# Kernel tuning notes

Measured on AMD Instinct MI355X. Metric: run time of the kernel, lower is better.

The kernel has to match this reference:

```python
import jax, jax.numpy as jnp
import numpy as np

N, INPUT_DIM, DIM, K, M_BOOK = 8192, 256, 128, 8192, 8
EPS = 1e-5  # torch BatchNorm1d default eps


def _bn(h, g, b, rm, rv):
    # eval-mode BatchNorm1d with running stats (dropout is identity in eval)
    return (h - rm) / jnp.sqrt(rv + EPS) * g + b


def setup_inputs() -> dict:
    key = jax.random.key(0)
    ks = jax.random.split(key, 20)
    s = 0.02
    inp = {
        "x": jax.random.normal(ks[0], (N, INPUT_DIM), jnp.float32),
        # encoder: input_dim -> 128 -> 256 -> dim
        "W1": jax.random.normal(ks[1], (INPUT_DIM, 128), jnp.float32) * s,
        "b1": jnp.zeros((128,), jnp.float32),
        "g1": jnp.ones((128,), jnp.float32),
        "be1": jnp.zeros((128,), jnp.float32),
        "rm1": jax.random.normal(ks[2], (128,), jnp.float32) * 0.1,
        "rv1": jax.random.uniform(ks[3], (128,), jnp.float32, 0.5, 1.5),
        "W2": jax.random.normal(ks[4], (128, 256), jnp.float32) * s,
        "b2": jnp.zeros((256,), jnp.float32),
        "g2": jnp.ones((256,), jnp.float32),
        "be2": jnp.zeros((256,), jnp.float32),
        "rm2": jax.random.normal(ks[5], (256,), jnp.float32) * 0.1,
        "rv2": jax.random.uniform(ks[6], (256,), jnp.float32, 0.5, 1.5),
        "W3": jax.random.normal(ks[7], (256, DIM), jnp.float32) * s,
        "b3": jnp.zeros((DIM,), jnp.float32),
        # m_book codebooks, torch init uniform(-1/K, 1/K)
        "codebooks": jax.random.uniform(ks[8], (M_BOOK, K, DIM), jnp.float32, -1.0 / K, 1.0 / K),
        # decoder: dim -> 256 -> 128 -> input_dim
        "W4": jax.random.normal(ks[9], (DIM, 256), jnp.float32) * s,
        "b4": jnp.zeros((256,), jnp.float32),
        "g3": jnp.ones((256,), jnp.float32),
        "be3": jnp.zeros((256,), jnp.float32),
        "rm3": jax.random.normal(ks[10], (256,), jnp.float32) * 0.1,
        "rv3": jax.random.uniform(ks[11], (256,), jnp.float32, 0.5, 1.5),
        "W5": jax.random.normal(ks[12], (256, 128), jnp.float32) * s,
        "b5": jnp.zeros((128,), jnp.float32),
        "g4": jnp.ones((128,), jnp.float32),
        "be4": jnp.zeros((128,), jnp.float32),
        "rm4": jax.random.normal(ks[13], (128,), jnp.float32) * 0.1,
        "rv4": jax.random.uniform(ks[14], (128,), jnp.float32, 0.5, 1.5),
        "W6": jax.random.normal(ks[15], (128, INPUT_DIM), jnp.float32) * s,
        "b6": jnp.zeros((INPUT_DIM,), jnp.float32),
    }
    return inp


def reference(x, W1, b1, g1, be1, rm1, rv1, W2, b2, g2, be2, rm2, rv2, W3, b3,
              codebooks, W4, b4, g3, be3, rm3, rv3, W5, b5, g4, be4, rm4, rv4, W6, b6):
    # encoder
    h = jax.nn.relu(_bn(x @ W1 + b1, g1, be1, rm1, rv1))
    h = jax.nn.relu(_bn(h @ W2 + b2, g2, be2, rm2, rv2))
    ze = h @ W3 + b3  # [N, DIM]

    # residual VQ over m_book codebooks
    def step(res, E):  # res [N, C], E [K, C]
        # squared distance ||e - r||^2 = ||r||^2 - 2 r.e + ||e||^2 (no [N,K,C] broadcast)
        d = (jnp.sum(res * res, axis=1, keepdims=True)
             - 2.0 * (res @ E.T)
             + jnp.sum(E * E, axis=1)[None, :])  # [N, K]
        idx = jnp.argmin(d, axis=1)  # [N]
        ce = E[idx]  # [N, C]
        return res - ce, (res, ce)

    _, (res_s, ce_s) = jax.lax.scan(step, ze, codebooks)  # each [M_BOOK, N, DIM]
    zq = jnp.sum(ce_s, axis=0)  # [N, DIM]

    # straight-through estimator
    di = ze + jax.lax.stop_gradient(zq - ze)

    # decoder
    h = jax.nn.relu(_bn(di @ W4 + b4, g3, be3, rm3, rv3))
    h = jax.nn.relu(_bn(h @ W5 + b5, g4, be4, rm4, rv4))
    x_hat = h @ W6 + b6  # [N, INPUT_DIM]
    return x_hat, res_s, ce_s
```

## Files before the change

### kernel.cpp

```cpp
#include <hip/hip_runtime.h>
#include <hip/hip_bf16.h>


typedef __bf16 bf16x8 __attribute__((ext_vector_type(8)));
typedef float  f32x4  __attribute__((ext_vector_type(4)));
typedef unsigned short ushort8v __attribute__((ext_vector_type(8)));

#define MFMA16(a,b,c) __builtin_amdgcn_mfma_f32_16x16x32_bf16((a),(b),(c),0,0,0)

__device__ __forceinline__ float b2f(ushort u){ return __uint_as_float(((unsigned)u) << 16); }
__device__ __forceinline__ ushort f2b_rne(float x){
  unsigned u = __float_as_uint(x);
  return (ushort)((u + 0x7fffu + ((u >> 16) & 1u)) >> 16);
}

__device__ __forceinline__ void cvt8(const float* p, bf16x8& h8, bf16x8& l8){
  f32x4 v0 = *(const f32x4*)p;
  f32x4 v1 = *(const f32x4*)(p + 4);
  ushort8v uh, ul;
  #pragma unroll
  for (int i = 0; i < 4; i++){
    float a = v0[i]; ushort h = f2b_rne(a); uh[i] = h;     ul[i]     = f2b_rne(a - b2f(h));
    float b = v1[i]; ushort g = f2b_rne(b); uh[i + 4] = g; ul[i + 4] = f2b_rne(b - b2f(g));
  }
  h8 = __builtin_bit_cast(bf16x8, uh);
  l8 = __builtin_bit_cast(bf16x8, ul);
}

template<int KK, int NN, bool HAS_BLO>
__device__ __forceinline__ f32x4 dotct(const bf16x8* ah, const bf16x8* al,
                                       const ushort* __restrict__ Bfh,
                                       const ushort* __restrict__ Bfl,
                                       int ct, int L){
  constexpr int KS = KK / 32, CT = NN / 16;
  f32x4 acc = {0.f, 0.f, 0.f, 0.f};
  #pragma unroll
  for (int ks = 0; ks < KS; ks++){
    int bo = ((ks * CT + ct) * 64 + L) * 8;
    bf16x8 bh = *(const bf16x8*)(Bfh + bo);
    acc = MFMA16(ah[ks], bh, acc);
    acc = MFMA16(al[ks], bh, acc);
    if constexpr (HAS_BLO){
      bf16x8 bl = *(const bf16x8*)(Bfl + bo);
      acc = MFMA16(ah[ks], bl, acc);
    }
  }
  return acc;
}

__device__ __forceinline__ void ebook_body(const float* __restrict__ Ef, ushort* __restrict__ Eb,
                                           float* __restrict__ hen, int code, int L){
  float2 e2 = *(const float2*)(Ef + code * 128 + L * 2);
  ushort h0 = f2b_rne(e2.x), h1 = f2b_rne(e2.y);
  int d = L * 2;
  int o = ((((code >> 4) * 4 + (d >> 5)) * 4 + ((d >> 3) & 3)) * 16 + (code & 15)) * 8 + (d & 7);
  *(unsigned*)(Eb + o) = (unsigned)h0 | ((unsigned)h1 << 16);
  float eh0 = b2f(h0), eh1 = b2f(h1);
  float s = eh0 * eh0 + eh1 * eh1;
  #pragma unroll
  for (int mask = 1; mask <= 32; mask <<= 1) s += __shfl_xor(s, mask);
  if (L == 0) hen[code] = 0.5f * s;
}

__device__ __forceinline__ void swz_body(const float* __restrict__ Wm, ushort* __restrict__ Wfh,
                                         ushort* __restrict__ Wfl, int N, int b){
  int gid = b * 256 + threadIdx.x;
  int k = gid / N, n = gid - k * N;
  int kt = k >> 5, kr = k & 31, nt = n >> 4, nr = n & 15;
  int lane = (kr >> 3) * 16 + nr, tt = kr & 7;
  int o = (((kt * (N >> 4)) + nt) * 64 + lane) * 8 + tt;
  float v = Wm[gid];
  ushort h = f2b_rne(v);
  Wfh[o] = h;
  if (Wfl) Wfl[o] = f2b_rne(v - b2f(h));
}

__global__ __launch_bounds__(256) void k_prep(
    const float* __restrict__ W1, const float* __restrict__ W2, const float* __restrict__ W3,
    const float* __restrict__ W4, const float* __restrict__ W5, const float* __restrict__ W6,
    ushort* W1fh, ushort* W1fl, ushort* W2fh, ushort* W2fl, ushort* W3fh, ushort* W3fl,
    ushort* W4fh, ushort* W5fh, ushort* W6fh,
    const float* __restrict__ CB, ushort* __restrict__ Eb, float* __restrict__ hen,
    const float* g1,const float* be1,const float* rm1,const float* rv1,
    const float* g2,const float* be2,const float* rm2,const float* rv2,
    const float* g3,const float* be3,const float* rm3,const float* rv3,
    const float* g4,const float* be4,const float* rm4,const float* rv4,
    float* s1,float* t1,float* s2,float* t2,float* s3,float* t3,float* s4,float* t4)
{
  int b = blockIdx.x;
  if (b < 768){
    if      (b < 128) swz_body(W1, W1fh, W1fl, 128, b);
    else if (b < 256) swz_body(W2, W2fh, W2fl, 256, b - 128);
    else if (b < 384) swz_body(W3, W3fh, W3fl, 128, b - 256);
    else if (b < 512) swz_body(W4, W4fh, nullptr, 256, b - 384);
    else if (b < 640) swz_body(W5, W5fh, nullptr, 128, b - 512);
    else              swz_body(W6, W6fh, nullptr, 256, b - 640);
  } else if (b == 768){
    int t = threadIdx.x;
    if (t < 128){
      float sa = g1[t] / sqrtf(rv1[t] + 1e-5f);
      s1[t] = sa; t1[t] = be1[t] - rm1[t] * sa;
      float sb = g4[t] / sqrtf(rv4[t] + 1e-5f);
      s4[t] = sb; t4[t] = be4[t] - rm4[t] * sb;
    }
    if (t < 256){
      float sa = g2[t] / sqrtf(rv2[t] + 1e-5f);
      s2[t] = sa; t2[t] = be2[t] - rm2[t] * sa;
      float sb = g3[t] / sqrtf(rv3[t] + 1e-5f);
      s3[t] = sb; t3[t] = be3[t] - rm3[t] * sb;
    }
  } else {
    ebook_body(CB, Eb, hen, (b - 769) * 4 + (threadIdx.x >> 6), threadIdx.x & 63);
  }
}

__global__ __launch_bounds__(256) void k_encoder(
    const float* __restrict__ x,
    const ushort* __restrict__ W1fh, const ushort* __restrict__ W1fl,
    const ushort* __restrict__ W2fh, const ushort* __restrict__ W2fl,
    const ushort* __restrict__ W3fh, const ushort* __restrict__ W3fl,
    const float* __restrict__ b1, const float* __restrict__ s1, const float* __restrict__ t1,
    const float* __restrict__ b2, const float* __restrict__ s2, const float* __restrict__ t2,
    const float* __restrict__ b3,
    ushort* __restrict__ rhi, float* __restrict__ res)
{
  __shared__ __align__(16) float sA[16 * 260];
  __shared__ __align__(16) float sB[16 * 132];
  int tid = threadIdx.x;
  int wv = tid >> 6, L = tid & 63;
  int qd = L >> 4, c16 = L & 15;
  int row0 = blockIdx.x * 16;

  bf16x8 a1h[8], a1l[8];
  #pragma unroll
  for (int ks = 0; ks < 8; ks++)
    cvt8(x + (row0 + c16) * 256 + ks * 32 + qd * 8, a1h[ks], a1l[ks]);

  #pragma unroll
  for (int u = 0; u < 2; u++){
    int ct = wv * 2 + u;
    f32x4 acc = dotct<256,128,true>(a1h, a1l, W1fh, W1fl, ct, L);
    int col = ct * 16 + c16;
    float bia = b1[col], sc = s1[col], sh = t1[col];
    #pragma unroll
    for (int i = 0; i < 4; i++){
      float v = (acc[i] + bia) * sc + sh;
      sB[(qd * 4 + i) * 132 + col] = fmaxf(v, 0.f);
    }
  }
  __syncthreads();

  bf16x8 a2h[4], a2l[4];
  #pragma unroll
  for (int ks = 0; ks < 4; ks++)
    cvt8(sB + c16 * 132 + ks * 32 + qd * 8, a2h[ks], a2l[ks]);

  #pragma unroll
  for (int u = 0; u < 4; u++){
    int ct = wv * 4 + u;
    f32x4 acc = dotct<128,256,true>(a2h, a2l, W2fh, W2fl, ct, L);
    int col = ct * 16 + c16;
    float bia = b2[col], sc = s2[col], sh = t2[col];
    #pragma unroll
    for (int i = 0; i < 4; i++){
      float v = (acc[i] + bia) * sc + sh;
      sA[(qd * 4 + i) * 260 + col] = fmaxf(v, 0.f);
    }
  }
  __syncthreads();

  bf16x8 a3h[8], a3l[8];
  #pragma unroll
  for (int ks = 0; ks < 8; ks++)
    cvt8(sA + c16 * 260 + ks * 32 + qd * 8, a3h[ks], a3l[ks]);

  #pragma unroll
  for (int u = 0; u < 2; u++){
    int ct = wv * 2 + u;
    f32x4 acc = dotct<256,128,true>(a3h, a3l, W3fh, W3fl, ct, L);
    int col = ct * 16 + c16;
    float bia = b3[col];
    #pragma unroll
    for (int i = 0; i < 4; i++){
      int row = row0 + qd * 4 + i;
      float v = acc[i] + bia;
      int o = row * 128 + col;
      res[o] = v;
      rhi[o] = f2b_rne(v);
    }
  }
}

__global__ __launch_bounds__(256) void k_decoder(
    const ushort* __restrict__ dhi, const ushort* __restrict__ dlo,
    const ushort* __restrict__ W4fh, const ushort* __restrict__ W5fh,
    const ushort* __restrict__ W6fh,
    const float* __restrict__ b4, const float* __restrict__ s3, const float* __restrict__ t3,
    const float* __restrict__ b5, const float* __restrict__ s4, const float* __restrict__ t4,
    const float* __restrict__ b6,
    float* __restrict__ xhat)
{
  __shared__ __align__(16) float sA[16 * 260];
  __shared__ __align__(16) float sB[16 * 132];
  int tid = threadIdx.x;
  int wv = tid >> 6, L = tid & 63;
  int qd = L >> 4, c16 = L & 15;
  int row0 = blockIdx.x * 16;

  bf16x8 a1h[4], a1l[4];
  #pragma unroll
  for (int ks = 0; ks < 4; ks++){
    int off = (row0 + c16) * 128 + ks * 32 + qd * 8;
    a1h[ks] = *(const bf16x8*)(dhi + off);
    a1l[ks] = *(const bf16x8*)(dlo + off);
  }

  #pragma unroll
  for (int u = 0; u < 4; u++){
    int ct = wv * 4 + u;
    f32x4 acc = dotct<128,256,false>(a1h, a1l, W4fh, nullptr, ct, L);
    int col = ct * 16 + c16;
    float bia = b4[col], sc = s3[col], sh = t3[col];
    #pragma unroll
    for (int i = 0; i < 4; i++){
      float v = (acc[i] + bia) * sc + sh;
      sA[(qd * 4 + i) * 260 + col] = fmaxf(v, 0.f);
    }
  }
  __syncthreads();

  bf16x8 a2h[8], a2l[8];
  #pragma unroll
  for (int ks = 0; ks < 8; ks++)
    cvt8(sA + c16 * 260 + ks * 32 + qd * 8, a2h[ks], a2l[ks]);

  #pragma unroll
  for (int u = 0; u < 2; u++){
    int ct = wv * 2 + u;
    f32x4 acc = dotct<256,128,false>(a2h, a2l, W5fh, nullptr, ct, L);
    int col = ct * 16 + c16;
    float bia = b5[col], sc = s4[col], sh = t4[col];
    #pragma unroll
    for (int i = 0; i < 4; i++){
      float v = (acc[i] + bia) * sc + sh;
      sB[(qd * 4 + i) * 132 + col] = fmaxf(v, 0.f);
    }
  }
  __syncthreads();

  bf16x8 a3h[4], a3l[4];
  #pragma unroll
  for (int ks = 0; ks < 4; ks++)
    cvt8(sB + c16 * 132 + ks * 32 + qd * 8, a3h[ks], a3l[ks]);

  #pragma unroll
  for (int u = 0; u < 4; u++){
    int ct = wv * 4 + u;
    f32x4 acc = dotct<128,256,false>(a3h, a3l, W6fh, nullptr, ct, L);
    int col = ct * 16 + c16;
    float bia = b6[col];
    #pragma unroll
    for (int i = 0; i < 4; i++)
      xhat[(row0 + qd * 4 + i) * 256 + col] = acc[i] + bia;
  }
}

__global__ __launch_bounds__(256, 4) void k_vq_argmin(
  const ushort* __restrict__ Rhi,
  const ushort* __restrict__ Eb, const float* __restrict__ hen,
  float* __restrict__ cq, int* __restrict__ cj)
{
  __shared__ __align__(16) ushort etile[2][8192];
  __shared__ float henl[512];
  int rb = blockIdx.x & 63, ch = blockIdx.x >> 6;
  int tid = threadIdx.x;
  int wv = tid >> 6, L = tid & 63;
  int qd = L >> 4, c16 = L & 15;
  int row0 = rb * 128 + wv * 32;

  bf16x8 ah[2][4];
  #pragma unroll
  for (int t = 0; t < 2; t++){
    int r = row0 + t * 16 + c16;
    #pragma unroll
    for (int ks = 0; ks < 4; ks++)
      ah[t][ks] = *(const bf16x8*)(Rhi + r * 128 + ks * 32 + qd * 8);
  }
  henl[tid] = hen[ch * 512 + tid];
  henl[tid + 256] = hen[ch * 512 + 256 + tid];

  float best[2][4]; int bj[2][4];
  #pragma unroll
  for (int t = 0; t < 2; t++)
    #pragma unroll
    for (int i = 0; i < 4; i++){ best[t][i] = -3.0e38f; bj[t][i] = 0; }

  const ushort* ebc = Eb + (size_t)ch * 65536;
  int jb = ch * 512 + c16;

  {
    const ushort* src = ebc + tid * 8;
    f32x4 v0 = *(const f32x4*)(src + 0 * 2048);
    f32x4 v1 = *(const f32x4*)(src + 1 * 2048);
    f32x4 v2 = *(const f32x4*)(src + 2 * 2048);
    f32x4 v3 = *(const f32x4*)(src + 3 * 2048);
    *(f32x4*)(etile[0] + 0 * 2048 + tid * 8) = v0;
    *(f32x4*)(etile[0] + 1 * 2048 + tid * 8) = v1;
    *(f32x4*)(etile[0] + 2 * 2048 + tid * 8) = v2;
    *(f32x4*)(etile[0] + 3 * 2048 + tid * 8) = v3;
  }
  __syncthreads();

  #pragma unroll 1
  for (int tile = 0; tile < 8; ++tile){
    int cur = tile & 1;
    f32x4 v0, v1, v2, v3;
    if (tile < 7){
      const ushort* src = ebc + (tile + 1) * 8192 + tid * 8;
      v0 = *(const f32x4*)(src + 0 * 2048);
      v1 = *(const f32x4*)(src + 1 * 2048);
      v2 = *(const f32x4*)(src + 2 * 2048);
      v3 = *(const f32x4*)(src + 3 * 2048);
    }
    const ushort* lb = etile[cur];
    #pragma unroll
    for (int g = 0; g < 4; ++g){
      const ushort* gp = lb + g * 2048 + L * 8;
      bf16x8 b0 = *(const bf16x8*)(gp + 0);
      bf16x8 b1 = *(const bf16x8*)(gp + 512);
      bf16x8 b2 = *(const bf16x8*)(gp + 1024);
      bf16x8 b3 = *(const bf16x8*)(gp + 1536);
      int gg = tile * 4 + g;
      float mh = -henl[gg * 16 + c16];
      f32x4 a0 = {mh, mh, mh, mh}, a1 = {mh, mh, mh, mh};
      __builtin_amdgcn_s_setprio(1);
      a0 = MFMA16(ah[0][0], b0, a0); a1 = MFMA16(ah[1][0], b0, a1);
      a0 = MFMA16(ah[0][1], b1, a0); a1 = MFMA16(ah[1][1], b1, a1);
      a0 = MFMA16(ah[0][2], b2, a0); a1 = MFMA16(ah[1][2], b2, a1);
      a0 = MFMA16(ah[0][3], b3, a0); a1 = MFMA16(ah[1][3], b3, a1);
      __builtin_amdgcn_s_setprio(0);
      int jc = jb + gg * 16;
      #pragma unroll
      for (int i = 0; i < 4; i++){
        if (a0[i] > best[0][i]){ best[0][i] = a0[i]; bj[0][i] = jc; }
        if (a1[i] > best[1][i]){ best[1][i] = a1[i]; bj[1][i] = jc; }
      }
    }
    if (tile < 7){
      ushort* nb = etile[cur ^ 1];
      *(f32x4*)(nb + 0 * 2048 + tid * 8) = v0;
      *(f32x4*)(nb + 1 * 2048 + tid * 8) = v1;
      *(f32x4*)(nb + 2 * 2048 + tid * 8) = v2;
      *(f32x4*)(nb + 3 * 2048 + tid * 8) = v3;
    }
    __syncthreads();
  }

  #pragma unroll
  for (int mask = 1; mask <= 8; mask <<= 1){
    #pragma unroll
    for (int t = 0; t < 2; t++)
      #pragma unroll
      for (int i = 0; i < 4; i++){
        float ob = __shfl_xor(best[t][i], mask);
        int   oj = __shfl_xor(bj[t][i], mask);
        if (ob > best[t][i] || (ob == best[t][i] && oj < bj[t][i])){ best[t][i] = ob; bj[t][i] = oj; }
      }
  }
  if (c16 == 0){
    #pragma unroll
    for (int t = 0; t < 2; t++)
      #pragma unroll
      for (int i = 0; i < 4; i++){
        int r = row0 + t * 16 + qd * 4 + i;
        cq[r * 16 + ch] = best[t][i];
        cj[r * 16 + ch] = bj[t][i];
      }
  }
}

template<bool LAST>
__global__ __launch_bounds__(256) void k_vq_update(
  const float* __restrict__ cq, const int* __restrict__ cj,
  const float* __restrict__ Ef, const float* __restrict__ Efn,
  ushort* __restrict__ Eb, float* __restrict__ hen,
  float* __restrict__ res, const float* __restrict__ ze_s,
  ushort* __restrict__ rhi, ushort* __restrict__ rlo,
  float* __restrict__ res_s, float* __restrict__ ce_s)
{
  int idx = blockIdx.x * 4 + (threadIdx.x >> 6);
  int L = threadIdx.x & 63;
  int c = L & 15;
  float bq = cq[idx * 16 + c]; int bi = cj[idx * 16 + c];
  #pragma unroll
  for (int mask = 1; mask <= 8; mask <<= 1){
    float ob = __shfl_xor(bq, mask);
    int   oj = __shfl_xor(bi, mask);
    if (ob > bq || (ob == bq && oj < bi)){ bq = ob; bi = oj; }
  }
  int o = idx * 128 + L * 2;
  float2 ce = *(const float2*)(Ef + bi * 128 + L * 2);
  float2 r2 = *(const float2*)(res + o);
  *(float2*)(res_s + o) = r2;
  *(float2*)(ce_s + o) = ce;
  float rn0 = r2.x - ce.x, rn1 = r2.y - ce.y;
  if constexpr (LAST){
    float2 z2 = *(const float2*)(ze_s + o);
    float d0 = z2.x - rn0, d1 = z2.y - rn1;
    ushort h0 = f2b_rne(d0), h1 = f2b_rne(d1);
    *(unsigned*)(rhi + o) = (unsigned)h0 | ((unsigned)h1 << 16);
    ushort l0 = f2b_rne(d0 - b2f(h0)), l1 = f2b_rne(d1 - b2f(h1));
    *(unsigned*)(rlo + o) = (unsigned)l0 | ((unsigned)l1 << 16);
  } else {
    res[o] = rn0; res[o + 1] = rn1;
    ushort h0 = f2b_rne(rn0), h1 = f2b_rne(rn1);
    *(unsigned*)(rhi + o) = (unsigned)h0 | ((unsigned)h1 << 16);
    ebook_body(Efn, Eb, hen, idx, L);
  }
}

extern "C" void kernel_launch(void* const* d_in, const int* in_sizes, int n_in,
                              void* d_out, int out_size, void* d_ws, size_t ws_size,
                              hipStream_t stream)
{
  const float* x   = (const float*)d_in[0];
  const float* W1  = (const float*)d_in[1];
  const float* b1  = (const float*)d_in[2];
  const float* g1  = (const float*)d_in[3];
  const float* be1 = (const float*)d_in[4];
  const float* rm1 = (const float*)d_in[5];
  const float* rv1 = (const float*)d_in[6];
  const float* W2  = (const float*)d_in[7];
  const float* b2  = (const float*)d_in[8];
  const float* g2  = (const float*)d_in[9];
  const float* be2 = (const float*)d_in[10];
  const float* rm2 = (const float*)d_in[11];
  const float* rv2 = (const float*)d_in[12];
  const float* W3  = (const float*)d_in[13];
  const float* b3  = (const float*)d_in[14];
  const float* CB  = (const float*)d_in[15];
  const float* W4  = (const float*)d_in[16];
  const float* b4  = (const float*)d_in[17];
  const float* g3  = (const float*)d_in[18];
  const float* be3 = (const float*)d_in[19];
  const float* rm3 = (const float*)d_in[20];
  const float* rv3 = (const float*)d_in[21];
  const float* W5  = (const float*)d_in[22];
  const float* b5  = (const float*)d_in[23];
  const float* g4  = (const float*)d_in[24];
  const float* be4 = (const float*)d_in[25];
  const float* rm4 = (const float*)d_in[26];
  const float* rv4 = (const float*)d_in[27];
  const float* W6  = (const float*)d_in[28];
  const float* b6  = (const float*)d_in[29];

  char* w = (char*)d_ws;
  ushort* Eb   = (ushort*)(w + 0);
  float*  cq   = (float*) (w + 2097152);
  int*    cj   = (int*)   (w + 2621440);
  ushort* rhi  = (ushort*)(w + 12582912);
  ushort* rlo  = (ushort*)(w + 14680064);
  float*  res  = (float*) (w + 16777216);
  float*  hen  = (float*) (w + 25165824);
  float*  s1   = (float*) (w + 25198592);
  float*  t1   = (float*) (w + 25199104);
  float*  s2   = (float*) (w + 25199616);
  float*  t2   = (float*) (w + 25200640);
  float*  s3   = (float*) (w + 25201664);
  float*  t3   = (float*) (w + 25202688);
  float*  s4   = (float*) (w + 25203712);
  float*  t4   = (float*) (w + 25204224);
  ushort* W1fh = (ushort*)(w + 25204736);
  ushort* W2fh = (ushort*)(w + 25270272);
  ushort* W3fh = (ushort*)(w + 25335808);
  ushort* W4fh = (ushort*)(w + 25401344);
  ushort* W5fh = (ushort*)(w + 25466880);
  ushort* W6fh = (ushort*)(w + 25532416);
  ushort* W1fl = (ushort*)(w + 25597952);
  ushort* W2fl = (ushort*)(w + 25663488);
  ushort* W3fl = (ushort*)(w + 25729024);

  float* xhat  = (float*)d_out;
  float* res_s = xhat + 2097152;
  float* ce_s  = res_s + 8388608;

  k_prep<<<2817, 256, 0, stream>>>(W1, W2, W3, W4, W5, W6,
                                   W1fh, W1fl, W2fh, W2fl, W3fh, W3fl,
                                   W4fh, W5fh, W6fh,
                                   CB, Eb, hen,
                                   g1,be1,rm1,rv1, g2,be2,rm2,rv2,
                                   g3,be3,rm3,rv3, g4,be4,rm4,rv4,
                                   s1,t1,s2,t2,s3,t3,s4,t4);

  k_encoder<<<512, 256, 0, stream>>>(x, W1fh, W1fl, W2fh, W2fl, W3fh, W3fl,
                                     b1, s1, t1, b2, s2, t2, b3,
                                     rhi, res);

  for (int m = 0; m < 8; m++){
    const float* Ef = CB + (size_t)m * 1048576;
    k_vq_argmin<<<1024, 256, 0, stream>>>(rhi, Eb, hen, cq, cj);
    if (m < 7){
      k_vq_update<false><<<2048, 256, 0, stream>>>(cq, cj, Ef, Ef + 1048576, Eb, hen,
                                                   res, nullptr, rhi, nullptr,
                                                   res_s + (size_t)m * 1048576,
                                                   ce_s  + (size_t)m * 1048576);
    } else {
      k_vq_update<true><<<2048, 256, 0, stream>>>(cq, cj, Ef, nullptr, Eb, hen,
                                                  res, res_s , rhi, rlo,
                                                  res_s + (size_t)m * 1048576,
                                                  ce_s  + (size_t)m * 1048576);
    }
  }

  k_decoder<<<512, 256, 0, stream>>>(rhi, rlo, W4fh, W5fh, W6fh,
                                     b4, s3, t3, b5, s4, t4, b6, xhat);
}
```

Before: 416.7 us.

## Switch VQ argmin to 32x32 MFMA tiles with direct global-to-LDS codebook loads

The VQ argmin kernel moves from 16x16x32 MFMA on two row tiles to a single 32x32x16 MFMA per 32-code group. The codebook bf16 swizzle layout changes to match, and the double-buffered codebook tiles are now fetched with global_load_lds instead of passing through registers. The aim is fewer LDS fragment reads and fewer argmin compares per MFMA, plus lower VGPR pressure. In exchange the butterfly reduction grows to 5 levels over 16 accumulators, and the async LDS fill has to be correctly synchronised before use.

```diff
diff --git a/kernel.cpp b/kernel.cpp
--- a/kernel.cpp
+++ b/kernel.cpp
@@ -4,14 +4,22 @@
 
 typedef __bf16 bf16x8 __attribute__((ext_vector_type(8)));
 typedef float  f32x4  __attribute__((ext_vector_type(4)));
+typedef float  f32x16 __attribute__((ext_vector_type(16)));
 typedef unsigned short ushort8v __attribute__((ext_vector_type(8)));
 
 #define MFMA16(a,b,c) __builtin_amdgcn_mfma_f32_16x16x32_bf16((a),(b),(c),0,0,0)
+#define MFMA32(a,b,c) __builtin_amdgcn_mfma_f32_32x32x16_bf16((a),(b),(c),0,0,0)
 
 __device__ __forceinline__ float b2f(ushort u){ return __uint_as_float(((unsigned)u) << 16); }
 __device__ __forceinline__ ushort f2b_rne(float x){
   unsigned u = __float_as_uint(x);
   return (ushort)((u + 0x7fffu + ((u >> 16) & 1u)) >> 16);
+}
+
+__device__ __forceinline__ void gload_lds16(const void* g, void* l){
+  __builtin_amdgcn_global_load_lds(
+      (const __attribute__((address_space(1))) unsigned int*)g,
+      (__attribute__((address_space(3))) unsigned int*)l, 16, 0, 0);
 }
 
 __device__ __forceinline__ void cvt8(const float* p, bf16x8& h8, bf16x8& l8){
@@ -53,7 +61,7 @@
   float2 e2 = *(const float2*)(Ef + code * 128 + L * 2);
   ushort h0 = f2b_rne(e2.x), h1 = f2b_rne(e2.y);
   int d = L * 2;
-  int o = ((((code >> 4) * 4 + (d >> 5)) * 4 + ((d >> 3) & 3)) * 16 + (code & 15)) * 8 + (d & 7);
+  int o = ((code >> 5) * 8 + (d >> 4)) * 512 + ((d >> 3) & 1) * 256 + (code & 31) * 8 + (d & 7);
   *(unsigned*)(Eb + o) = (unsigned)h0 | ((unsigned)h1 << 16);
   float eh0 = b2f(h0), eh1 = b2f(h1);
   float s = eh0 * eh0 + eh1 * eh1;
@@ -275,107 +283,92 @@
   int rb = blockIdx.x & 63, ch = blockIdx.x >> 6;
   int tid = threadIdx.x;
   int wv = tid >> 6, L = tid & 63;
-  int qd = L >> 4, c16 = L & 15;
+  int c32 = L & 31, lh = L >> 5;
   int row0 = rb * 128 + wv * 32;
 
-  bf16x8 ah[2][4];
-  #pragma unroll
-  for (int t = 0; t < 2; t++){
-    int r = row0 + t * 16 + c16;
-    #pragma unroll
-    for (int ks = 0; ks < 4; ks++)
-      ah[t][ks] = *(const bf16x8*)(Rhi + r * 128 + ks * 32 + qd * 8);
-  }
+  bf16x8 ah[8];
+  #pragma unroll
+  for (int ks = 0; ks < 8; ks++)
+    ah[ks] = *(const bf16x8*)(Rhi + (row0 + c32) * 128 + ks * 16 + lh * 8);
+
   henl[tid] = hen[ch * 512 + tid];
   henl[tid + 256] = hen[ch * 512 + 256 + tid];
 
-  float best[2][4]; int bj[2][4];
-  #pragma unroll
-  for (int t = 0; t < 2; t++)
-    #pragma unroll
-    for (int i = 0; i < 4; i++){ best[t][i] = -3.0e38f; bj[t][i] = 0; }
+  float best[16]; int bj[16];
+  #pragma unroll
+  for (int i = 0; i < 16; i++){ best[i] = -3.0e38f; bj[i] = 0; }
 
   const ushort* ebc = Eb + (size_t)ch * 65536;
-  int jb = ch * 512 + c16;
-
-  {
-    const ushort* src = ebc + tid * 8;
-    f32x4 v0 = *(const f32x4*)(src + 0 * 2048);
-    f32x4 v1 = *(const f32x4*)(src + 1 * 2048);
-    f32x4 v2 = *(const f32x4*)(src + 2 * 2048);
-    f32x4 v3 = *(const f32x4*)(src + 3 * 2048);
-    *(f32x4*)(etile[0] + 0 * 2048 + tid * 8) = v0;
-    *(f32x4*)(etile[0] + 1 * 2048 + tid * 8) = v1;
-    *(f32x4*)(etile[0] + 2 * 2048 + tid * 8) = v2;
-    *(f32x4*)(etile[0] + 3 * 2048 + tid * 8) = v3;
-  }
+  int jb = ch * 512 + c32;
+
+  #pragma unroll
+  for (int j = 0; j < 4; j++)
+    gload_lds16(ebc + j * 2048 + wv * 512 + L * 8, etile[0] + j * 4096 + wv * 512);
   __syncthreads();
 
   #pragma unroll 1
   for (int tile = 0; tile < 8; ++tile){
     int cur = tile & 1;
-    f32x4 v0, v1, v2, v3;
     if (tile < 7){
-      const ushort* src = ebc + (tile + 1) * 8192 + tid * 8;
-      v0 = *(const f32x4*)(src + 0 * 2048);
-      v1 = *(const f32x4*)(src + 1 * 2048);
-      v2 = *(const f32x4*)(src + 2 * 2048);
-      v3 = *(const f32x4*)(src + 3 * 2048);
+      const ushort* src = ebc + (size_t)(tile + 1) * 8192;
+      ushort* nb = etile[cur ^ 1];
+      #pragma unroll
+      for (int j = 0; j < 4; j++)
+        gload_lds16(src + j * 2048 + wv * 512 + L * 8, nb + j * 4096 + wv * 512);
     }
     const ushort* lb = etile[cur];
     #pragma unroll
-    for (int g = 0; g < 4; ++g){
-      const ushort* gp = lb + g * 2048 + L * 8;
+    for (int g = 0; g < 2; ++g){
+      const ushort* gp = lb + g * 4096 + L * 8;
+      int gg = tile * 2 + g;
+      float mh = -henl[gg * 32 + c32];
+      f32x16 acc;
+      #pragma unroll
+      for (int i = 0; i < 16; i++) acc[i] = mh;
       bf16x8 b0 = *(const bf16x8*)(gp + 0);
       bf16x8 b1 = *(const bf16x8*)(gp + 512);
       bf16x8 b2 = *(const bf16x8*)(gp + 1024);
       bf16x8 b3 = *(const bf16x8*)(gp + 1536);
-      int gg = tile * 4 + g;
-      float mh = -henl[gg * 16 + c16];
-      f32x4 a0 = {mh, mh, mh, mh}, a1 = {mh, mh, mh, mh};
       __builtin_amdgcn_s_setprio(1);
-      a0 = MFMA16(ah[0][0], b0, a0); a1 = MFMA16(ah[1][0], b0, a1);
-      a0 = MFMA16(ah[0][1], b1, a0); a1 = MFMA16(ah[1][1], b1, a1);
-      a0 = MFMA16(ah[0][2], b2, a0); a1 = MFMA16(ah[1][2], b2, a1);
-      a0 = MFMA16(ah[0][3], b3, a0); a1 = MFMA16(ah[1][3], b3, a1);
+      acc = MFMA32(ah[0], b0, acc);
+      acc = MFMA32(ah[1], b1, acc);
+      acc = MFMA32(ah[2], b2, acc);
+      acc = MFMA32(ah[3], b3, acc);
       __builtin_amdgcn_s_setprio(0);
-      int jc = jb + gg * 16;
+      bf16x8 b4 = *(const bf16x8*)(gp + 2048);
+      bf16x8 b5 = *(const bf16x8*)(gp + 2560);
+      bf16x8 b6 = *(const bf16x8*)(gp + 3072);
+      bf16x8 b7 = *(const bf16x8*)(gp + 3584);
+      __builtin_amdgcn_s_setprio(1);
+      acc = MFMA32(ah[4], b4, acc);
+      acc = MFMA32(ah[5], b5, acc);
+      acc = MFMA32(ah[6], b6, acc);
+      acc = MFMA32(ah[7], b7, acc);
+      __builtin_amdgcn_s_setprio(0);
+      int jc = jb + gg * 32;
       #pragma unroll
-      for (int i = 0; i < 4; i++){
-        if (a0[i] > best[0][i]){ best[0][i] = a0[i]; bj[0][i] = jc; }
-        if (a1[i] > best[1][i]){ best[1][i] = a1[i]; bj[1][i] = jc; }
-      }
-    }
-    if (tile < 7){
-      ushort* nb = etile[cur ^ 1];
-      *(f32x4*)(nb + 0 * 2048 + tid * 8) = v0;
-      *(f32x4*)(nb + 1 * 2048 + tid * 8) = v1;
-      *(f32x4*)(nb + 2 * 2048 + tid * 8) = v2;
-      *(f32x4*)(nb + 3 * 2048 + tid * 8) = v3;
+      for (int i = 0; i < 16; i++)
+        if (acc[i] > best[i]){ best[i] = acc[i]; bj[i] = jc; }
     }
     __syncthreads();
   }
 
   #pragma unroll
-  for (int mask = 1; mask <= 8; mask <<= 1){
-    #pragma unroll
-    for (int t = 0; t < 2; t++)
-      #pragma unroll
-      for (int i = 0; i < 4; i++){
-        float ob = __shfl_xor(best[t][i], mask);
-        int   oj = __shfl_xor(bj[t][i], mask);
-        if (ob > best[t][i] || (ob == best[t][i] && oj < bj[t][i])){ best[t][i] = ob; bj[t][i] = oj; }
-      }
-  }
-  if (c16 == 0){
-    #pragma unroll
-    for (int t = 0; t < 2; t++)
-      #pragma unroll
-      for (int i = 0; i < 4; i++){
-        int r = row0 + t * 16 + qd * 4 + i;
-        cq[r * 16 + ch] = best[t][i];
-        cj[r * 16 + ch] = bj[t][i];
-      }
+  for (int mask = 1; mask <= 16; mask <<= 1){
+    #pragma unroll
+    for (int i = 0; i < 16; i++){
+      float ob = __shfl_xor(best[i], mask);
+      int   oj = __shfl_xor(bj[i], mask);
+      if (ob > best[i] || (ob == best[i] && oj < bj[i])){ best[i] = ob; bj[i] = oj; }
+    }
+  }
+  if (c32 == 0){
+    #pragma unroll
+    for (int i = 0; i < 16; i++){
+      int r = row0 + (i & 3) + 8 * (i >> 2) + 4 * lh;
+      cq[r * 16 + ch] = best[i];
+      cj[r * 16 + ch] = bj[i];
+    }
   }
 }
 
```

New measurement: 467.9 us. +12.3%, slower.
